# Optimization experiments

Measured on AMD Instinct MI355X. Metric: run time of the kernel, lower is better.

## Reference

```python
import jax, jax.numpy as jnp
import numpy as np

B, D, P = 4096, 1024, 64
CHILDREN = (16, 32)  # num_children_per_parent


def setup_inputs() -> dict:
    key = jax.random.key(0)
    ks = jax.random.split(key, 8)
    std = 2e-05  # trunc_normal std from the torch init (plain normal is fine at this tiny std)
    x = jax.random.normal(ks[0], (B, D), dtype=jnp.float32)
    parent_w = jax.random.normal(ks[1], (P, D), dtype=jnp.float32) * std
    parent_b = jnp.zeros((P,), dtype=jnp.float32)
    child_w0 = jax.random.normal(ks[2], (P, CHILDREN[0], D), dtype=jnp.float32) * std
    child_b0 = jnp.zeros((P, CHILDREN[0]), dtype=jnp.float32)
    child_w1 = jax.random.normal(ks[3], (P, CHILDREN[1], D), dtype=jnp.float32) * std
    child_b1 = jnp.zeros((P, CHILDREN[1]), dtype=jnp.float32)
    return {"x": x, "parent_w": parent_w, "parent_b": parent_b,
            "child_w0": child_w0, "child_b0": child_b0,
            "child_w1": child_w1, "child_b1": child_b1}


def reference(x, parent_w, parent_b, child_w0, child_b0, child_w1, child_b1):
    # head_drop with p=0.0 / eval mode -> identity
    parent_logits = x @ parent_w.T + parent_b            # [B, P]
    parent_probs = jax.nn.softmax(parent_logits, axis=1)
    parent_class = jnp.argmax(parent_probs, axis=1)      # [B] top-1 routing

    # Grouped per-sample linear: gather the selected parent's child head, apply to x.
    w0 = child_w0[parent_class]                          # [B, C0, D]
    b0 = child_b0[parent_class]                          # [B, C0]
    c0 = jnp.einsum('bd,bcd->bc', x, w0) + b0            # [B, C0]

    w1 = child_w1[parent_class]                          # [B, C1, D]
    b1 = child_b1[parent_class]                          # [B, C1]
    c1 = jnp.einsum('bd,bcd->bc', x, w1) + b1            # [B, C1]

    return (parent_logits, c0, c1)
```

## Files before the change

kernel.cpp:

```cpp
#include <hip/hip_runtime.h>
#include <hip/hip_bf16.h>

#define B_N   4096
#define D_N   1024
#define P_N   64
#define C0_N  16
#define C1_N  32
#define NC_N  48

#define PRR   8
#define PKC   8
#define PDK   128

#define KC2   8
#define DKC2  128
#define TRC   64

#define GAP_TAU 1e-6f
#define NEG_INF (-3.402823466e38f)


typedef __attribute__((ext_vector_type(8))) short short8v;
typedef __attribute__((ext_vector_type(4))) float f32x4;

static __device__ __forceinline__ unsigned f2bf(float f) {
    union { float f; unsigned u; } v; v.f = f;
    return (v.u + 0x7FFF + ((v.u >> 16) & 1)) >> 16;
}
static __device__ __forceinline__ void split4(float4 v, uint2& hp, uint2& lp) {
    const unsigned hx = f2bf(v.x), hy = f2bf(v.y);
    const unsigned hz = f2bf(v.z), hw = f2bf(v.w);
    union { unsigned u; float f; } t;
    float rx, ry, rz, rw;
    t.u = hx << 16; rx = v.x - t.f;
    t.u = hy << 16; ry = v.y - t.f;
    t.u = hz << 16; rz = v.z - t.f;
    t.u = hw << 16; rw = v.w - t.f;
    hp.x = hx | (hy << 16);             hp.y = hz | (hw << 16);
    lp.x = f2bf(rx) | (f2bf(ry) << 16); lp.y = f2bf(rz) | (f2bf(rw) << 16);
}

__global__ __launch_bounds__(256, 3)
void hc_parent_fused(const float* __restrict__ x,
                     const float* __restrict__ pw,
                     const float* __restrict__ pb,
                     float* __restrict__ out_logits,
                     float* __restrict__ out_cz,
                     int* __restrict__ pclass) {
    __shared__ unsigned short xh[16][17][8], xl[16][17][8];
    __shared__ unsigned short wh[16][65][8], wl[16][65][8];
    __shared__ float  llds[PRR][68];
    __shared__ double ld[P_N];
    __shared__ int    sq[PRR];
    __shared__ int    sqn;

    const int tid = threadIdx.x;
    const int r0  = blockIdx.x * PRR;

    if (tid == 0) sqn = 0;
    if (tid < 96)
        ((float4*)(out_cz + (size_t)blockIdx.x * (PRR * NC_N)))[tid] =
            make_float4(0.f, 0.f, 0.f, 0.f);

    const int lane = tid & 63;
    const int wv   = tid >> 6;
    const int lr   = lane & 15;
    const int lg   = lane >> 4;

    f32x4 acc = {0.f, 0.f, 0.f, 0.f};

    for (int kc = 0; kc < PKC; ++kc) {
        const int d0 = kc * PDK;
        __syncthreads();
        {
            const int r = tid >> 5, c4 = (tid & 31) * 4;
            const float4 v = *(const float4*)&x[(size_t)(r0 + r) * D_N + d0 + c4];
            uint2 hp, lp; split4(v, hp, lp);
            *(uint2*)&xh[c4 >> 3][r][c4 & 4] = hp;
            *(uint2*)&xl[c4 >> 3][r][c4 & 4] = lp;
        }
        #pragma unroll
        for (int k = 0; k < 8; ++k) {
            const int f = tid + 256 * k, r = f >> 5, c4 = (f & 31) * 4;
            const float4 v = *(const float4*)&pw[(size_t)r * D_N + d0 + c4];
            uint2 hp, lp; split4(v, hp, lp);
            *(uint2*)&wh[c4 >> 3][r][c4 & 4] = hp;
            *(uint2*)&wl[c4 >> 3][r][c4 & 4] = lp;
        }
        __syncthreads();

        #pragma unroll
        for (int ks = 0; ks < 4; ++ks) {
            const int kq = ks * 4 + lg;
            const short8v ah = *(const short8v*)&xh[kq][lr][0];
            const short8v al = *(const short8v*)&xl[kq][lr][0];
            const short8v bh = *(const short8v*)&wh[kq][wv * 16 + lr][0];
            const short8v bl = *(const short8v*)&wl[kq][wv * 16 + lr][0];
            acc = __builtin_amdgcn_mfma_f32_16x16x32_bf16(ah, bh, acc, 0, 0, 0);
            acc = __builtin_amdgcn_mfma_f32_16x16x32_bf16(al, bh, acc, 0, 0, 0);
            acc = __builtin_amdgcn_mfma_f32_16x16x32_bf16(ah, bl, acc, 0, 0, 0);
        }
    }
    __syncthreads();
    if (lg < 2) {
        #pragma unroll
        for (int reg = 0; reg < 4; ++reg)
            llds[lg * 4 + reg][wv * 16 + lr] = acc[reg];
    }
    __syncthreads();

    const int p = lane;
    #pragma unroll
    for (int rq = 0; rq < 2; ++rq) {
        const int rloc = wv * 2 + rq;
        const int row  = r0 + rloc;
        const float l  = llds[rloc][p] + pb[p];
        out_logits[(size_t)row * P_N + p] = l;

        float m1 = l; int i1 = p; float m2 = NEG_INF;
        #pragma unroll
        for (int off = 32; off > 0; off >>= 1) {
            const float om1 = __shfl_xor(m1, off);
            const int   oi1 = __shfl_xor(i1, off);
            const float om2 = __shfl_xor(m2, off);
            if (om1 > m1 || (om1 == m1 && oi1 < i1)) {
                m2 = fmaxf(m1, om2); m1 = om1; i1 = oi1;
            } else m2 = fmaxf(m2, om1);
        }
        if (p == 0) {
            if (m1 - m2 > GAP_TAU) {
                pclass[row] = i1;
            } else {
                const int q = atomicAdd(&sqn, 1);
                sq[q] = row;
            }
        }
    }
    __syncthreads();

    const int nq = sqn;
    if (nq == 0) return;

    for (int qi = 0; qi < nq; ++qi) {
        const int srow = sq[qi];
        const float* xr = &x[(size_t)srow * D_N + p * 16];
        float4 xv[4];
        #pragma unroll
        for (int k = 0; k < 4; ++k) xv[k] = *(const float4*)&xr[k * 4];

        #pragma unroll 2
        for (int pass = 0; pass < 16; ++pass) {
            const int pp = wv * 16 + pass;
            const float* wr = &pw[(size_t)pp * D_N + p * 16];
            double a0 = 0.0, a1 = 0.0, a2 = 0.0, a3 = 0.0;
            #pragma unroll
            for (int k = 0; k < 4; ++k) {
                const float4 wv2 = *(const float4*)&wr[k * 4];
                a0 = fma((double)wv2.x, (double)xv[k].x, a0);
                a1 = fma((double)wv2.y, (double)xv[k].y, a1);
                a2 = fma((double)wv2.z, (double)xv[k].z, a2);
                a3 = fma((double)wv2.w, (double)xv[k].w, a3);
            }
            double a = (a0 + a1) + (a2 + a3);
            #pragma unroll
            for (int off = 32; off > 0; off >>= 1) a += __shfl_xor(a, off);
            if (p == 0) ld[pp] = a;
        }
        __syncthreads();

        if (wv == 0) {
            const double accv = (double)pb[p] + ld[p];
            const float  l32  = (float)accv;
            float m = l32;
            #pragma unroll
            for (int off = 32; off > 0; off >>= 1)
                m = fmaxf(m, __shfl_xor(m, off));
            const float e = (float)exp((double)(l32 - m));
            double es = (double)e;
            #pragma unroll
            for (int off = 32; off > 0; off >>= 1) es += __shfl_xor(es, off);
            es = __shfl(es, 0);
            const float s    = (float)es;
            const float prob = e / s;
            float pm = prob; int pi = p;
            #pragma unroll
            for (int off = 32; off > 0; off >>= 1) {
                const float opm = __shfl_xor(pm, off);
                const int   opi = __shfl_xor(pi, off);
                if (opm > pm || (opm == pm && opi < pi)) { pm = opm; pi = opi; }
            }
            if (p == 0) pclass[srow] = pi;
        }
        __syncthreads();
    }
}

__global__ __launch_bounds__(256, 5)
void hc_child_mfma(const float* __restrict__ x,
                   const float* __restrict__ w0,
                   const float* __restrict__ w1,
                   const float* __restrict__ b0,
                   const float* __restrict__ b1,
                   const int* __restrict__ pclass,
                   float* __restrict__ out_c0,
                   float* __restrict__ out_c1) {
    const int c  = blockIdx.x;
    const int kc = blockIdx.y;
    const int t0 = blockIdx.z * TRC;
    const int d0 = kc * DKC2;

    __shared__ int            scnt[256];
    __shared__ int            slist[TRC];
    __shared__ unsigned short xs[16][TRC][8];
    __shared__ unsigned short ws[16][NC_N][8];

    const int tid = threadIdx.x;

    const int rbase = tid * 16;
    int myc = 0;
    #pragma unroll
    for (int k = 0; k < 16; ++k)
        myc += (pclass[rbase + k] == c) ? 1 : 0;
    scnt[tid] = myc;
    __syncthreads();
    for (int off = 1; off < 256; off <<= 1) {
        const int v = scnt[tid];
        const int u = (tid >= off) ? scnt[tid - off] : 0;
        __syncthreads();
        scnt[tid] = v + u;
        __syncthreads();
    }
    const int excl = scnt[tid] - myc;
    const int n    = scnt[255];
    if (t0 >= n) return;
    const int m = min(TRC, n - t0);
    {
        int pos = excl;
        #pragma unroll
        for (int k = 0; k < 16; ++k) {
            const int row = rbase + k;
            if (pclass[row] == c) {
                const int rel = pos - t0;
                if (rel >= 0 && rel < TRC) slist[rel] = row;
                ++pos;
            }
        }
    }
    __syncthreads();

    #pragma unroll
    for (int k = 0; k < 6; ++k) {
        const int f = tid + 256 * k, j = f >> 5, c4 = (f & 31) * 4;
        const float* src = (j < C0_N)
            ? &w0[((size_t)c * C0_N + j) * D_N + d0 + c4]
            : &w1[((size_t)c * C1_N + (j - C0_N)) * D_N + d0 + c4];
        const float4 v = *(const float4*)src;
        unsigned short* dst = &ws[c4 >> 3][j][c4 & 4];
        dst[0] = (unsigned short)f2bf(v.x); dst[1] = (unsigned short)f2bf(v.y);
        dst[2] = (unsigned short)f2bf(v.z); dst[3] = (unsigned short)f2bf(v.w);
    }
    #pragma unroll
    for (int k = 0; k < 8; ++k) {
        const int f = tid + 256 * k, r = f >> 5, c4 = (f & 31) * 4;
        const int row = slist[r < m ? r : 0];
        const float4 v = *(const float4*)&x[(size_t)row * D_N + d0 + c4];
        unsigned short* dst = &xs[c4 >> 3][r][c4 & 4];
        dst[0] = (unsigned short)f2bf(v.x); dst[1] = (unsigned short)f2bf(v.y);
        dst[2] = (unsigned short)f2bf(v.z); dst[3] = (unsigned short)f2bf(v.w);
    }
    __syncthreads();

    const int lane = tid & 63;
    const int wv   = tid >> 6;
    const int lr   = lane & 15;
    const int lg   = lane >> 4;

    f32x4 acc0 = {0.f, 0.f, 0.f, 0.f};
    f32x4 acc1 = {0.f, 0.f, 0.f, 0.f};
    f32x4 acc2 = {0.f, 0.f, 0.f, 0.f};
    #pragma unroll
    for (int ks = 0; ks < 4; ++ks) {
        const int kq = ks * 4 + lg;
        const short8v a  = *(const short8v*)&xs[kq][wv * 16 + lr][0];
        const short8v bA = *(const short8v*)&ws[kq][lr][0];
        const short8v bB = *(const short8v*)&ws[kq][16 + lr][0];
        const short8v bC = *(const short8v*)&ws[kq][32 + lr][0];
        acc0 = __builtin_amdgcn_mfma_f32_16x16x32_bf16(a, bA, acc0, 0, 0, 0);
        acc1 = __builtin_amdgcn_mfma_f32_16x16x32_bf16(a, bB, acc1, 0, 0, 0);
        acc2 = __builtin_amdgcn_mfma_f32_16x16x32_bf16(a, bC, acc2, 0, 0, 0);
    }

    #pragma unroll
    for (int reg = 0; reg < 4; ++reg) {
        const int rr = wv * 16 + lg * 4 + reg;
        if (rr < m) {
            const int row = slist[rr];
            #pragma unroll
            for (int nt = 0; nt < 3; ++nt) {
                const int jj = nt * 16 + lr;
                float v = (nt == 0) ? acc0[reg] : (nt == 1) ? acc1[reg] : acc2[reg];
                if (kc == 0)
                    v += (jj < C0_N) ? b0[c * C0_N + jj]
                                     : b1[c * C1_N + (jj - C0_N)];
                if (jj < C0_N)
                    atomicAdd(&out_c0[(size_t)row * C0_N + jj], v);
                else
                    atomicAdd(&out_c1[(size_t)row * C1_N + (jj - C0_N)], v);
            }
        }
    }
}

extern "C" void kernel_launch(void* const* d_in, const int* in_sizes, int n_in,
                              void* d_out, int out_size, void* d_ws, size_t ws_size,
                              hipStream_t stream) {
    const float* x  = (const float*)d_in[0];
    const float* pw = (const float*)d_in[1];
    const float* pb = (const float*)d_in[2];
    const float* w0 = (const float*)d_in[3];
    const float* b0 = (const float*)d_in[4];
    const float* w1 = (const float*)d_in[5];
    const float* b1 = (const float*)d_in[6];

    float* out_logits = (float*)d_out;
    float* out_c0     = out_logits + (size_t)B_N * P_N;
    float* out_c1     = out_c0     + (size_t)B_N * C0_N;

    int* pclass = (int*)d_ws;

    hc_parent_fused<<<B_N / PRR, 256, 0, stream>>>(
        x, pw, pb, out_logits, out_c0, pclass);

    hc_child_mfma<<<dim3(P_N, KC2, 3), 256, 0, stream>>>(
        x, w0, w1, b0, b1, pclass, out_c0, out_c1);
}
```

Baseline: 44.52 us.

## Load MFMA operands directly from global memory, dropping LDS staging in parent GEMM

The parent-logit GEMM no longer stages x and parent weights through shared memory with block barriers. Each lane now loads its own 8-float fragments straight from global memory and splits them into bf16 hi/lo pairs in registers. The split now truncates instead of rounding to nearest, and occupancy is raised to 4 blocks per SM via launch bounds. This removes the LDS writes, reads and syncs, at the cost of redundant global reads: x rows are duplicated across lanes and waves, and each wave reads its weights separately. Truncation also slightly changes the hi/lo split, which may affect argmax near ties.

```diff
diff --git a/kernel.cpp b/kernel.cpp
--- a/kernel.cpp
+++ b/kernel.cpp
@@ -9,8 +9,6 @@
 #define NC_N  48
 
 #define PRR   8
-#define PKC   8
-#define PDK   128
 
 #define KC2   8
 #define DKC2  128
@@ -27,28 +25,29 @@
     union { float f; unsigned u; } v; v.f = f;
     return (v.u + 0x7FFF + ((v.u >> 16) & 1)) >> 16;
 }
-static __device__ __forceinline__ void split4(float4 v, uint2& hp, uint2& lp) {
-    const unsigned hx = f2bf(v.x), hy = f2bf(v.y);
-    const unsigned hz = f2bf(v.z), hw = f2bf(v.w);
-    union { unsigned u; float f; } t;
-    float rx, ry, rz, rw;
-    t.u = hx << 16; rx = v.x - t.f;
-    t.u = hy << 16; ry = v.y - t.f;
-    t.u = hz << 16; rz = v.z - t.f;
-    t.u = hw << 16; rw = v.w - t.f;
-    hp.x = hx | (hy << 16);             hp.y = hz | (hw << 16);
-    lp.x = f2bf(rx) | (f2bf(ry) << 16); lp.y = f2bf(rz) | (f2bf(rw) << 16);
-}
-
-__global__ __launch_bounds__(256, 3)
+
+static __device__ __forceinline__ void split8(float4 a, float4 b,
+                                              short8v& h, short8v& l) {
+    const float e[8] = {a.x, a.y, a.z, a.w, b.x, b.y, b.z, b.w};
+    #pragma unroll
+    for (int i = 0; i < 8; ++i) {
+        union { float f; unsigned u; } t, s;
+        t.f = e[i];
+        const unsigned hu = t.u >> 16;
+        s.u = hu << 16;
+        t.f = e[i] - s.f;
+        h[i] = (short)hu;
+        l[i] = (short)(t.u >> 16);
+    }
+}
+
+__global__ __launch_bounds__(256, 4)
 void hc_parent_fused(const float* __restrict__ x,
                      const float* __restrict__ pw,
                      const float* __restrict__ pb,
                      float* __restrict__ out_logits,
                      float* __restrict__ out_cz,
                      int* __restrict__ pclass) {
-    __shared__ unsigned short xh[16][17][8], xl[16][17][8];
-    __shared__ unsigned short wh[16][65][8], wl[16][65][8];
     __shared__ float  llds[PRR][68];
     __shared__ double ld[P_N];
     __shared__ int    sq[PRR];
@@ -67,41 +66,24 @@
     const int lr   = lane & 15;
     const int lg   = lane >> 4;
 
+    const float* xbase = &x[(size_t)(r0 + (lr & 7)) * D_N + lg * 8];
+    const float* wbase = &pw[(size_t)(wv * 16 + lr) * D_N + lg * 8];
+
     f32x4 acc = {0.f, 0.f, 0.f, 0.f};
-
-    for (int kc = 0; kc < PKC; ++kc) {
-        const int d0 = kc * PDK;
-        __syncthreads();
-        {
-            const int r = tid >> 5, c4 = (tid & 31) * 4;
-            const float4 v = *(const float4*)&x[(size_t)(r0 + r) * D_N + d0 + c4];
-            uint2 hp, lp; split4(v, hp, lp);
-            *(uint2*)&xh[c4 >> 3][r][c4 & 4] = hp;
-            *(uint2*)&xl[c4 >> 3][r][c4 & 4] = lp;
-        }
-        #pragma unroll
-        for (int k = 0; k < 8; ++k) {
-            const int f = tid + 256 * k, r = f >> 5, c4 = (f & 31) * 4;
-            const float4 v = *(const float4*)&pw[(size_t)r * D_N + d0 + c4];
-            uint2 hp, lp; split4(v, hp, lp);
-            *(uint2*)&wh[c4 >> 3][r][c4 & 4] = hp;
-            *(uint2*)&wl[c4 >> 3][r][c4 & 4] = lp;
-        }
-        __syncthreads();
-
-        #pragma unroll
-        for (int ks = 0; ks < 4; ++ks) {
-            const int kq = ks * 4 + lg;
-            const short8v ah = *(const short8v*)&xh[kq][lr][0];
-            const short8v al = *(const short8v*)&xl[kq][lr][0];
-            const short8v bh = *(const short8v*)&wh[kq][wv * 16 + lr][0];
-            const short8v bl = *(const short8v*)&wl[kq][wv * 16 + lr][0];
-            acc = __builtin_amdgcn_mfma_f32_16x16x32_bf16(ah, bh, acc, 0, 0, 0);
-            acc = __builtin_amdgcn_mfma_f32_16x16x32_bf16(al, bh, acc, 0, 0, 0);
-            acc = __builtin_amdgcn_mfma_f32_16x16x32_bf16(ah, bl, acc, 0, 0, 0);
-        }
-    }
-    __syncthreads();
+    #pragma unroll 4
+    for (int ks = 0; ks < 32; ++ks) {
+        const float4 xa = *(const float4*)&xbase[ks * 32];
+        const float4 xb = *(const float4*)&xbase[ks * 32 + 4];
+        const float4 wa = *(const float4*)&wbase[ks * 32];
+        const float4 wb = *(const float4*)&wbase[ks * 32 + 4];
+        short8v ah, al, bh, bl;
+        split8(xa, xb, ah, al);
+        split8(wa, wb, bh, bl);
+        acc = __builtin_amdgcn_mfma_f32_16x16x32_bf16(ah, bh, acc, 0, 0, 0);
+        acc = __builtin_amdgcn_mfma_f32_16x16x32_bf16(al, bh, acc, 0, 0, 0);
+        acc = __builtin_amdgcn_mfma_f32_16x16x32_bf16(ah, bl, acc, 0, 0, 0);
+    }
+
     if (lg < 2) {
         #pragma unroll
         for (int reg = 0; reg < 4; ++reg)
```

Measured after the change: 59.43 us. 1.33x slower.
